# Kernel tuning notes

Measured on AMD Instinct MI355X. Metric: run time of the kernel, lower is better.

Reference implementation:

```python
import jax, jax.numpy as jnp
import numpy as np

B, T, D = 4, 8192, 512

def setup_inputs() -> dict:
    key = jax.random.key(0)
    k_x, k_w1, k_w2 = jax.random.split(key, 3)
    # Xavier-uniform-ish init for linear weights
    lim1 = np.sqrt(6.0 / (D + D)).astype(np.float32)
    lim2 = np.sqrt(6.0 / (D + 1)).astype(np.float32)
    return {
        "x": jax.random.normal(k_x, (B, T, D), dtype=jnp.float32),
        "W1": jax.random.uniform(k_w1, (D, D), dtype=jnp.float32, minval=-lim1, maxval=lim1),
        "b1": jnp.zeros((D,), dtype=jnp.float32),
        "w2": jax.random.uniform(k_w2, (D,), dtype=jnp.float32, minval=-lim2, maxval=lim2),
        "b2": jnp.zeros((), dtype=jnp.float32),
    }

def reference(x, W1, b1, w2, b2):
    h = jnp.tanh(jnp.einsum("btd,ed->bte", x, W1) + b1)   # [B,T,D]
    s = jnp.einsum("bte,e->bt", h, w2) + b2               # [B,T]
    # Causal prefix softmax-weighted sum:
    # context[b,t] = sum_{u<=t} softmax(s[b,:t+1])[u] * x[b,u]
    # Softmax is shift-invariant, so subtracting the global per-row max keeps
    # every prefix softmax exact while being numerically stable.
    m = jnp.max(s, axis=1, keepdims=True)                 # [B,1]
    e = jnp.exp(s - m)                                    # [B,T]
    den = jnp.cumsum(e, axis=1)                           # [B,T]
    num = jnp.cumsum(e[..., None] * x, axis=1)            # [B,T,D]
    context = num / den[..., None]                        # [B,T,D]
    return context
```

## Files before the change

### kernel.cpp

```cpp
#include <hip/hip_runtime.h>
#include <hip/hip_bf16.h>
#include <math.h>

#define BATCH 4
#define TLEN 8192
#define BT 32768
#define DIM 512
#define CHUNK 128
#define NCHUNK 64

#define BM 128
#define BN 128
#define BK 32

typedef _Float16 h8 __attribute__((ext_vector_type(8)));
typedef _Float16 h4 __attribute__((ext_vector_type(4)));
typedef float f4 __attribute__((ext_vector_type(4)));

__device__ __forceinline__ void gload_lds16(const _Float16* g, _Float16* l) {
    __builtin_amdgcn_global_load_lds(
        (const __attribute__((address_space(1))) void*)g,
        (__attribute__((address_space(3))) void*)l, 16, 0, 0);
}

__device__ __forceinline__ float fast_tanh(float z) {
    float u = __expf(2.0f * z);
    return 1.0f - __fdividef(2.0f, u + 1.0f);
}

__global__ __launch_bounds__(256) void convert_kernel(
    const float* __restrict__ x, const float* __restrict__ W1,
    _Float16* __restrict__ hbuf)
{
    const long i = (long)blockIdx.x * 256 + threadIdx.x;
    const long XD4 = (long)BT * DIM / 4;
    const long total4 = XD4 + (long)DIM * DIM / 4;
    if (i >= total4) return;
    float4 v;
    if (i < XD4) v = ((const float4*)x)[i];
    else         v = ((const float4*)W1)[i - XD4];
    h4 o = { (_Float16)v.x, (_Float16)v.y, (_Float16)v.z, (_Float16)v.w };
    *(h4*)(hbuf + i * 4) = o;
}

__global__ __launch_bounds__(256, 4) void score_mfma_kernel(
    const _Float16* __restrict__ xh, const _Float16* __restrict__ wh,
    const float* __restrict__ b1, const float* __restrict__ w2,
    float* __restrict__ spart)
{
    __shared__ _Float16 Als[2][BM * BK];
    __shared__ _Float16 Bls[2][BM * BK];
    __shared__ float sred[2][BM];

    const int orig = blockIdx.x;
    const int wid  = (orig & 7) * 128 + (orig >> 3);
    const int bt = wid >> 2, be = wid & 3;
    const long trow0 = (long)bt * BM;
    const int  ecol0 = be * BN;

    const int tid  = threadIdx.x;
    const int lane = tid & 63;
    const int w    = tid >> 6;
    const int wr   = w >> 1;
    const int wc   = w & 1;
    const int l15  = lane & 15;
    const int lg   = lane >> 4;

    const int srow = w * 32 + (lane >> 2);
    const int skof = ((lane & 3) ^ (srow & 3)) * 8;
    const _Float16* ga = xh + (trow0 + srow) * DIM + skof;
    const _Float16* gb = wh + (long)(ecol0 + srow) * DIM + skof;
    _Float16* laA0 = &Als[0][w * 1024];
    _Float16* laB0 = &Bls[0][w * 1024];
    _Float16* laA1 = &Als[1][w * 1024];
    _Float16* laB1 = &Bls[1][w * 1024];

    const int koff = (lg ^ (l15 & 3)) * 8;

    float b1v[4], w2v[4];
    #pragma unroll
    for (int n = 0; n < 4; ++n) {
        int e = ecol0 + wc * 64 + n * 16 + l15;
        b1v[n] = b1[e];
        w2v[n] = w2[e];
    }
    asm volatile("s_waitcnt vmcnt(0)" ::: "memory");

    f4 acc[4][4];
    #pragma unroll
    for (int m = 0; m < 4; ++m)
        #pragma unroll
        for (int n = 0; n < 4; ++n) acc[m][n] = (f4){0.f, 0.f, 0.f, 0.f};

#define STAGE(A_, B_, k0_) {                         \
    gload_lds16(ga + (k0_),            (A_));        \
    gload_lds16(ga + 16 * DIM + (k0_), (A_) + 512);  \
    gload_lds16(gb + (k0_),            (B_));        \
    gload_lds16(gb + 16 * DIM + (k0_), (B_) + 512);  }

#define COMPUTE(bsel_) {                                                      \
    h8 afr[4], bfr[4];                                                        \
    _Pragma("unroll")                                                         \
    for (int m = 0; m < 4; ++m)                                               \
        afr[m] = *(const h8*)&Als[bsel_][(wr * 64 + m * 16 + l15) * BK + koff]; \
    _Pragma("unroll")                                                         \
    for (int n = 0; n < 4; ++n)                                               \
        bfr[n] = *(const h8*)&Bls[bsel_][(wc * 64 + n * 16 + l15) * BK + koff]; \
    _Pragma("unroll")                                                         \
    for (int m = 0; m < 4; ++m)                                               \
        _Pragma("unroll")                                                     \
        for (int n = 0; n < 4; ++n)                                           \
            acc[m][n] = __builtin_amdgcn_mfma_f32_16x16x32_f16(               \
                afr[m], bfr[n], acc[m][n], 0, 0, 0);                          }

    STAGE(laA0, laB0, 0);
    #pragma unroll 2
    for (int s = 0; s < 15; ++s) {
        if (s & 1) { STAGE(laA0, laB0, (s + 1) * BK); }
        else       { STAGE(laA1, laB1, (s + 1) * BK); }
        asm volatile("s_waitcnt vmcnt(4)" ::: "memory");
        __builtin_amdgcn_s_barrier();
        if (s & 1) { COMPUTE(1); } else { COMPUTE(0); }
        asm volatile("s_waitcnt lgkmcnt(0)" ::: "memory");
        __builtin_amdgcn_s_barrier();
    }
    asm volatile("s_waitcnt vmcnt(0)" ::: "memory");
    __builtin_amdgcn_s_barrier();
    COMPUTE(1);

    float pp[4][4];
    #pragma unroll
    for (int m = 0; m < 4; ++m)
        #pragma unroll
        for (int i = 0; i < 4; ++i) {
            float p = 0.f;
            #pragma unroll
            for (int n = 0; n < 4; ++n)
                p += w2v[n] * fast_tanh(acc[m][n][i] + b1v[n]);
            pp[m][i] = p;
        }
    #pragma unroll
    for (int off = 1; off < 16; off <<= 1)
        #pragma unroll
        for (int m = 0; m < 4; ++m)
            #pragma unroll
            for (int i = 0; i < 4; ++i)
                pp[m][i] += __shfl_xor(pp[m][i], off);
    __syncthreads();
    if (l15 == 0) {
        #pragma unroll
        for (int m = 0; m < 4; ++m)
            #pragma unroll
            for (int i = 0; i < 4; ++i)
                sred[wc][wr * 64 + m * 16 + lg * 4 + i] = pp[m][i];
    }
    __syncthreads();
    if (tid < BM)
        spart[(long)be * BT + trow0 + tid] = sred[0][tid] + sred[1][tid];
}

__global__ __launch_bounds__(128) void chunk_sum_kernel(
    const _Float16* __restrict__ xh, const float* __restrict__ spart,
    float* __restrict__ s_ws, float* __restrict__ csum,
    float* __restrict__ esum)
{
    __shared__ float el[CHUNK];
    __shared__ float wred[2];
    const int c = blockIdx.x, b = blockIdx.y;
    const int tid = threadIdx.x;
    const long bt = (long)b * TLEN + c * CHUNK + tid;

    float sv = spart[bt] + spart[BT + bt] + spart[2l * BT + bt] + spart[3l * BT + bt];
    s_ws[bt] = sv;
    float ev = __expf(sv);
    el[tid] = ev;
    float r = ev;
    #pragma unroll
    for (int off = 1; off < 64; off <<= 1) r += __shfl_xor(r, off);
    if ((tid & 63) == 0) wred[tid >> 6] = r;
    __syncthreads();
    if (tid == 0) esum[b * NCHUNK + c] = wred[0] + wred[1];

    const _Float16* xb = xh + ((long)b * TLEN + c * CHUNK) * DIM;
    float a0 = 0.f, a1 = 0.f, a2 = 0.f, a3 = 0.f;
    for (int t = 0; t < CHUNK; ++t) {
        h4 xv = *(const h4*)(xb + (long)t * DIM + tid * 4);
        float wgt = el[t];
        a0 += wgt * (float)xv[0];
        a1 += wgt * (float)xv[1];
        a2 += wgt * (float)xv[2];
        a3 += wgt * (float)xv[3];
    }
    float4 o = {a0, a1, a2, a3};
    ((float4*)(csum + ((long)(b * NCHUNK + c)) * DIM))[tid] = o;
}

__global__ __launch_bounds__(576) void chunk_scan_kernel(
    float* __restrict__ csum, float* __restrict__ esum)
{
    const int b = blockIdx.x;
    const int tid = threadIdx.x;
    if (tid < 512) {
        const int d = tid;
        float run = 0.f;
        #pragma unroll 8
        for (int c = 0; c < NCHUNK; ++c) {
            float* p = csum + ((long)(b * NCHUNK + c)) * DIM + d;
            float v = *p;
            *p = run;
            run += v;
        }
    } else {
        const int lane = tid - 512;
        float v = esum[b * NCHUNK + lane];
        const float own = v;
        #pragma unroll
        for (int off = 1; off < 64; off <<= 1) {
            float u = __shfl_up(v, off);
            if (lane >= off) v += u;
        }
        esum[b * NCHUNK + lane] = v - own;
    }
}

__global__ __launch_bounds__(128) void context_kernel(
    const float* __restrict__ x, const float* __restrict__ s_ws,
    const float* __restrict__ esum, const float* __restrict__ csum,
    float* __restrict__ out)
{
    __shared__ float el[CHUNK];
    const int c = blockIdx.x, b = blockIdx.y;
    const int tid = threadIdx.x;
    el[tid] = __expf(s_ws[(long)b * TLEN + c * CHUNK + tid]);
    __syncthreads();
    float dacc = esum[b * NCHUNK + c];
    const float4* xb = (const float4*)(x + ((long)b * TLEN + c * CHUNK) * DIM);
    float4* ob = (float4*)(out + ((long)b * TLEN + c * CHUNK) * DIM);
    float4 acc = ((const float4*)(csum + ((long)(b * NCHUNK + c)) * DIM))[tid];
    for (int t = 0; t < CHUNK; ++t) {
        float4 xv = xb[t * (DIM / 4) + tid];
        float wv = el[t];
        dacc += wv;
        acc.x += wv * xv.x; acc.y += wv * xv.y;
        acc.z += wv * xv.z; acc.w += wv * xv.w;
        float inv = __fdividef(1.0f, dacc);
        float4 o = {acc.x * inv, acc.y * inv, acc.z * inv, acc.w * inv};
        ob[t * (DIM / 4) + tid] = o;
    }
}

extern "C" void kernel_launch(void* const* d_in, const int* in_sizes, int n_in,
                              void* d_out, int out_size, void* d_ws, size_t ws_size,
                              hipStream_t stream)
{
    const float* x  = (const float*)d_in[0];
    const float* W1 = (const float*)d_in[1];
    const float* b1 = (const float*)d_in[2];
    const float* w2 = (const float*)d_in[3];
    float* out = (float*)d_out;

    float* ws   = (float*)d_ws;
    float* s_ws = ws;
    float* csum = ws + BT;
    float* esum = ws + BT + 4 * NCHUNK * DIM;

    _Float16* hbuf = (_Float16*)d_out;
    const _Float16* xh = hbuf;
    const _Float16* wh = hbuf + (long)BT * DIM;
    float* spart = (float*)(hbuf + (long)BT * DIM + DIM * DIM);

    const long total4 = ((long)BT * DIM + (long)DIM * DIM) / 4;
    const int convBlocks = (int)((total4 + 255) / 256);

    convert_kernel<<<convBlocks, 256, 0, stream>>>(x, W1, hbuf);
    score_mfma_kernel<<<(BT / BM) * 4, 256, 0, stream>>>(xh, wh, b1, w2, spart);
    chunk_sum_kernel<<<dim3(NCHUNK, BATCH), 128, 0, stream>>>(xh, spart, s_ws, csum, esum);
    chunk_scan_kernel<<<BATCH, 576, 0, stream>>>(csum, esum);
    context_kernel<<<dim3(NCHUNK, BATCH), 128, 0, stream>>>(x, s_ws, esum, csum, out);
}
```

Measured before the change: 83.47 us.

## Fuse fp32-to-fp16 conversion into score GEMM and drop separate convert pass

Removes the standalone convert kernel that wrote fp16 copies of x and W1, and instead has the score GEMM load fp32 tiles into registers, pack-convert them to fp16 and write them to shared memory with a new k-major layout. The main loop becomes register-prefetch plus compute plus convert-write with one barrier per step, replacing the async global-to-LDS path, and occupancy hint drops from 4 to 3. chunk_sum now reads fp32 x directly. This saves the full write and re-read of an fp16 copy of x, at the cost of doubled global read bytes in the GEMM and more register pressure.

```diff
diff --git a/kernel.cpp b/kernel.cpp
--- a/kernel.cpp
+++ b/kernel.cpp
@@ -14,42 +14,21 @@
 #define BK 32
 
 typedef _Float16 h8 __attribute__((ext_vector_type(8)));
-typedef _Float16 h4 __attribute__((ext_vector_type(4)));
+typedef __fp16 fp16x2 __attribute__((ext_vector_type(2)));
 typedef float f4 __attribute__((ext_vector_type(4)));
-
-__device__ __forceinline__ void gload_lds16(const _Float16* g, _Float16* l) {
-    __builtin_amdgcn_global_load_lds(
-        (const __attribute__((address_space(1))) void*)g,
-        (__attribute__((address_space(3))) void*)l, 16, 0, 0);
-}
 
 __device__ __forceinline__ float fast_tanh(float z) {
     float u = __expf(2.0f * z);
     return 1.0f - __fdividef(2.0f, u + 1.0f);
 }
 
-__global__ __launch_bounds__(256) void convert_kernel(
+__global__ __launch_bounds__(256, 3) void score_mfma_kernel(
     const float* __restrict__ x, const float* __restrict__ W1,
-    _Float16* __restrict__ hbuf)
-{
-    const long i = (long)blockIdx.x * 256 + threadIdx.x;
-    const long XD4 = (long)BT * DIM / 4;
-    const long total4 = XD4 + (long)DIM * DIM / 4;
-    if (i >= total4) return;
-    float4 v;
-    if (i < XD4) v = ((const float4*)x)[i];
-    else         v = ((const float4*)W1)[i - XD4];
-    h4 o = { (_Float16)v.x, (_Float16)v.y, (_Float16)v.z, (_Float16)v.w };
-    *(h4*)(hbuf + i * 4) = o;
-}
-
-__global__ __launch_bounds__(256, 4) void score_mfma_kernel(
-    const _Float16* __restrict__ xh, const _Float16* __restrict__ wh,
     const float* __restrict__ b1, const float* __restrict__ w2,
     float* __restrict__ spart)
 {
-    __shared__ _Float16 Als[2][BM * BK];
-    __shared__ _Float16 Bls[2][BM * BK];
+    __shared__ _Float16 Als[2][4 * 128 * 8];
+    __shared__ _Float16 Bls[2][4 * 128 * 8];
     __shared__ float sred[2][BM];
 
     const int orig = blockIdx.x;
@@ -66,16 +45,12 @@
     const int l15  = lane & 15;
     const int lg   = lane >> 4;
 
-    const int srow = w * 32 + (lane >> 2);
-    const int skof = ((lane & 3) ^ (srow & 3)) * 8;
-    const _Float16* ga = xh + (trow0 + srow) * DIM + skof;
-    const _Float16* gb = wh + (long)(ecol0 + srow) * DIM + skof;
-    _Float16* laA0 = &Als[0][w * 1024];
-    _Float16* laB0 = &Bls[0][w * 1024];
-    _Float16* laA1 = &Als[1][w * 1024];
-    _Float16* laB1 = &Bls[1][w * 1024];
-
-    const int koff = (lg ^ (l15 & 3)) * 8;
+    const int srow = w * 32 + (lane >> 1);
+    const int kgb  = (lane & 1) * 2;
+    const float* gA = x  + (trow0 + srow) * DIM + kgb * 8;
+    const float* gB = W1 + (long)(ecol0 + srow) * DIM + kgb * 8;
+    const int wof0 = kgb * 1024 + srow * 8;
+    const int wof1 = wof0 + 1024;
 
     float b1v[4], w2v[4];
     #pragma unroll
@@ -84,7 +59,6 @@
         b1v[n] = b1[e];
         w2v[n] = w2[e];
     }
-    asm volatile("s_waitcnt vmcnt(0)" ::: "memory");
 
     f4 acc[4][4];
     #pragma unroll
@@ -92,20 +66,49 @@
         #pragma unroll
         for (int n = 0; n < 4; ++n) acc[m][n] = (f4){0.f, 0.f, 0.f, 0.f};
 
-#define STAGE(A_, B_, k0_) {                         \
-    gload_lds16(ga + (k0_),            (A_));        \
-    gload_lds16(ga + 16 * DIM + (k0_), (A_) + 512);  \
-    gload_lds16(gb + (k0_),            (B_));        \
-    gload_lds16(gb + 16 * DIM + (k0_), (B_) + 512);  }
+    float4 a0_, a1_, a2_, a3_, b0_, b1_, b2_, b3_;
+
+#define LOADR(k0_) {                                                          \
+    a0_ = *(const float4*)(gA + (k0_));                                       \
+    a1_ = *(const float4*)(gA + (k0_) + 4);                                   \
+    a2_ = *(const float4*)(gA + (k0_) + 8);                                   \
+    a3_ = *(const float4*)(gA + (k0_) + 12);                                  \
+    b0_ = *(const float4*)(gB + (k0_));                                       \
+    b1_ = *(const float4*)(gB + (k0_) + 4);                                   \
+    b2_ = *(const float4*)(gB + (k0_) + 8);                                   \
+    b3_ = *(const float4*)(gB + (k0_) + 12);                                  }
+
+#define CVTWRITE(bsel_) {                                                     \
+    union { h8 v; fp16x2 p[4]; } uA0, uA1, uB0, uB1;                          \
+    uA0.p[0] = __builtin_amdgcn_cvt_pkrtz(a0_.x, a0_.y);                      \
+    uA0.p[1] = __builtin_amdgcn_cvt_pkrtz(a0_.z, a0_.w);                      \
+    uA0.p[2] = __builtin_amdgcn_cvt_pkrtz(a1_.x, a1_.y);                      \
+    uA0.p[3] = __builtin_amdgcn_cvt_pkrtz(a1_.z, a1_.w);                      \
+    uA1.p[0] = __builtin_amdgcn_cvt_pkrtz(a2_.x, a2_.y);                      \
+    uA1.p[1] = __builtin_amdgcn_cvt_pkrtz(a2_.z, a2_.w);                      \
+    uA1.p[2] = __builtin_amdgcn_cvt_pkrtz(a3_.x, a3_.y);                      \
+    uA1.p[3] = __builtin_amdgcn_cvt_pkrtz(a3_.z, a3_.w);                      \
+    uB0.p[0] = __builtin_amdgcn_cvt_pkrtz(b0_.x, b0_.y);                      \
+    uB0.p[1] = __builtin_amdgcn_cvt_pkrtz(b0_.z, b0_.w);                      \
+    uB0.p[2] = __builtin_amdgcn_cvt_pkrtz(b1_.x, b1_.y);                      \
+    uB0.p[3] = __builtin_amdgcn_cvt_pkrtz(b1_.z, b1_.w);                      \
+    uB1.p[0] = __builtin_amdgcn_cvt_pkrtz(b2_.x, b2_.y);                      \
+    uB1.p[1] = __builtin_amdgcn_cvt_pkrtz(b2_.z, b2_.w);                      \
+    uB1.p[2] = __builtin_amdgcn_cvt_pkrtz(b3_.x, b3_.y);                      \
+    uB1.p[3] = __builtin_amdgcn_cvt_pkrtz(b3_.z, b3_.w);                      \
+    *(h8*)&Als[bsel_][wof0] = uA0.v;                                          \
+    *(h8*)&Als[bsel_][wof1] = uA1.v;                                          \
+    *(h8*)&Bls[bsel_][wof0] = uB0.v;                                          \
+    *(h8*)&Bls[bsel_][wof1] = uB1.v;                                          }
 
 #define COMPUTE(bsel_) {                                                      \
     h8 afr[4], bfr[4];                                                        \
     _Pragma("unroll")                                                         \
     for (int m = 0; m < 4; ++m)                                               \
-        afr[m] = *(const h8*)&Als[bsel_][(wr * 64 + m * 16 + l15) * BK + koff]; \
+        afr[m] = *(const h8*)&Als[bsel_][lg * 1024 + (wr * 64 + m * 16 + l15) * 8]; \
     _Pragma("unroll")                                                         \
     for (int n = 0; n < 4; ++n)                                               \
-        bfr[n] = *(const h8*)&Bls[bsel_][(wc * 64 + n * 16 + l15) * BK + koff]; \
+        bfr[n] = *(const h8*)&Bls[bsel_][lg * 1024 + (wc * 64 + n * 16 + l15) * 8]; \
     _Pragma("unroll")                                                         \
     for (int m = 0; m < 4; ++m)                                               \
         _Pragma("unroll")                                                     \
@@ -113,19 +116,17 @@
             acc[m][n] = __builtin_amdgcn_mfma_f32_16x16x32_f16(               \
                 afr[m], bfr[n], acc[m][n], 0, 0, 0);                          }
 
-    STAGE(laA0, laB0, 0);
-    #pragma unroll 2
+    LOADR(0);
+    CVTWRITE(0);
+    __syncthreads();
+
+    #pragma unroll
     for (int s = 0; s < 15; ++s) {
-        if (s & 1) { STAGE(laA0, laB0, (s + 1) * BK); }
-        else       { STAGE(laA1, laB1, (s + 1) * BK); }
-        asm volatile("s_waitcnt vmcnt(4)" ::: "memory");
-        __builtin_amdgcn_s_barrier();
-        if (s & 1) { COMPUTE(1); } else { COMPUTE(0); }
-        asm volatile("s_waitcnt lgkmcnt(0)" ::: "memory");
-        __builtin_amdgcn_s_barrier();
-    }
-    asm volatile("s_waitcnt vmcnt(0)" ::: "memory");
-    __builtin_amdgcn_s_barrier();
+        LOADR((s + 1) * BK);
+        COMPUTE(s & 1);
+        CVTWRITE((s + 1) & 1);
+        __syncthreads();
+    }
     COMPUTE(1);
 
     float pp[4][4];
@@ -160,7 +161,7 @@
 }
 
 __global__ __launch_bounds__(128) void chunk_sum_kernel(
-    const _Float16* __restrict__ xh, const float* __restrict__ spart,
+    const float* __restrict__ x, const float* __restrict__ spart,
     float* __restrict__ s_ws, float* __restrict__ csum,
     float* __restrict__ esum)
 {
@@ -181,18 +182,15 @@
     __syncthreads();
     if (tid == 0) esum[b * NCHUNK + c] = wred[0] + wred[1];
 
-    const _Float16* xb = xh + ((long)b * TLEN + c * CHUNK) * DIM;
-    float a0 = 0.f, a1 = 0.f, a2 = 0.f, a3 = 0.f;
+    const float4* xb = (const float4*)(x + ((long)b * TLEN + c * CHUNK) * DIM);
+    float4 acc = {0.f, 0.f, 0.f, 0.f};
     for (int t = 0; t < CHUNK; ++t) {
-        h4 xv = *(const h4*)(xb + (long)t * DIM + tid * 4);
+        float4 xv = xb[t * (DIM / 4) + tid];
         float wgt = el[t];
-        a0 += wgt * (float)xv[0];
-        a1 += wgt * (float)xv[1];
-        a2 += wgt * (float)xv[2];
-        a3 += wgt * (float)xv[3];
-    }
-    float4 o = {a0, a1, a2, a3};
-    ((float4*)(csum + ((long)(b * NCHUNK + c)) * DIM))[tid] = o;
+        acc.x += wgt * xv.x; acc.y += wgt * xv.y;
+        acc.z += wgt * xv.z; acc.w += wgt * xv.w;
+    }
+    ((float4*)(csum + ((long)(b * NCHUNK + c)) * DIM))[tid] = acc;
 }
 
 __global__ __launch_bounds__(576) void chunk_scan_kernel(
@@ -264,17 +262,10 @@
     float* csum = ws + BT;
     float* esum = ws + BT + 4 * NCHUNK * DIM;
 
-    _Float16* hbuf = (_Float16*)d_out;
-    const _Float16* xh = hbuf;
-    const _Float16* wh = hbuf + (long)BT * DIM;
-    float* spart = (float*)(hbuf + (long)BT * DIM + DIM * DIM);
-
-    const long total4 = ((long)BT * DIM + (long)DIM * DIM) / 4;
-    const int convBlocks = (int)((total4 + 255) / 256);
-
-    convert_kernel<<<convBlocks, 256, 0, stream>>>(x, W1, hbuf);
-    score_mfma_kernel<<<(BT / BM) * 4, 256, 0, stream>>>(xh, wh, b1, w2, spart);
-    chunk_sum_kernel<<<dim3(NCHUNK, BATCH), 128, 0, stream>>>(xh, spart, s_ws, csum, esum);
+    float* spart = out + 12l * 1024 * 1024;
+
+    score_mfma_kernel<<<(BT / BM) * 4, 256, 0, stream>>>(x, W1, b1, w2, spart);
+    chunk_sum_kernel<<<dim3(NCHUNK, BATCH), 128, 0, stream>>>(x, spart, s_ws, csum, esum);
     chunk_scan_kernel<<<BATCH, 576, 0, stream>>>(csum, esum);
     context_kernel<<<dim3(NCHUNK, BATCH), 128, 0, stream>>>(x, s_ws, esum, csum, out);
 }
```

Result: slower. 87.07 us (+4.3%).

## Fuse chunk sum, scan and context into one cooperative kernel with LDS-staged x

Applied to the files above, without the earlier changes.

Replaces the separate chunk-sum, chunk-scan and context kernels with one cooperative kernel. Each block stages its fp16 x chunk in LDS, writes its per-chunk sums, waits at a grid-wide sync, then rebuilds its prefix offsets by summing earlier chunks' partials directly. The output pass reuses the LDS-resident fp16 x instead of re-reading fp32 x from global memory, which removes two launches and a full fp32 read of x. The trade-offs are a grid barrier, a large 128 KB LDS footprint per block, one block per CU, redundant prefix summation, and lower output precision because context is now built from fp16 x.

```diff
diff --git a/kernel.cpp b/kernel.cpp
--- a/kernel.cpp
+++ b/kernel.cpp
@@ -1,6 +1,9 @@
 #include <hip/hip_runtime.h>
 #include <hip/hip_bf16.h>
+#include <hip/hip_cooperative_groups.h>
 #include <math.h>
+
+namespace cg = cooperative_groups;
 
 #define BATCH 4
 #define TLEN 8192
@@ -15,6 +18,7 @@
 
 typedef _Float16 h8 __attribute__((ext_vector_type(8)));
 typedef _Float16 h4 __attribute__((ext_vector_type(4)));
+typedef _Float16 h2 __attribute__((ext_vector_type(2)));
 typedef float f4 __attribute__((ext_vector_type(4)));
 
 __device__ __forceinline__ void gload_lds16(const _Float16* g, _Float16* l) {
@@ -159,93 +163,78 @@
         spart[(long)be * BT + trow0 + tid] = sred[0][tid] + sred[1][tid];
 }
 
-__global__ __launch_bounds__(128) void chunk_sum_kernel(
+__global__ __launch_bounds__(256, 1) void fused_context_kernel(
     const _Float16* __restrict__ xh, const float* __restrict__ spart,
-    float* __restrict__ s_ws, float* __restrict__ csum,
-    float* __restrict__ esum)
-{
+    float* __restrict__ csum, float* __restrict__ esum,
+    float* __restrict__ out)
+{
+    __shared__ _Float16 xls[CHUNK * DIM];
     __shared__ float el[CHUNK];
     __shared__ float wred[2];
-    const int c = blockIdx.x, b = blockIdx.y;
+
+    cg::grid_group grid = cg::this_grid();
+
+    const int bid = blockIdx.x;
+    const int c = bid & (NCHUNK - 1);
+    const int b = bid >> 6;
     const int tid = threadIdx.x;
-    const long bt = (long)b * TLEN + c * CHUNK + tid;
-
-    float sv = spart[bt] + spart[BT + bt] + spart[2l * BT + bt] + spart[3l * BT + bt];
-    s_ws[bt] = sv;
-    float ev = __expf(sv);
-    el[tid] = ev;
-    float r = ev;
-    #pragma unroll
-    for (int off = 1; off < 64; off <<= 1) r += __shfl_xor(r, off);
-    if ((tid & 63) == 0) wred[tid >> 6] = r;
+    const long rowbase = (long)b * TLEN + c * CHUNK;
+
+    if (tid < CHUNK) {
+        const long bt = rowbase + tid;
+        float sv = spart[bt] + spart[BT + bt]
+                 + spart[2l * BT + bt] + spart[3l * BT + bt];
+        float ev = __expf(sv);
+        el[tid] = ev;
+        float r = ev;
+        #pragma unroll
+        for (int off = 1; off < 64; off <<= 1) r += __shfl_xor(r, off);
+        if ((tid & 63) == 0) wred[tid >> 6] = r;
+    }
+
+    {
+        const h8* g = (const h8*)(xh + rowbase * DIM);
+        h8* l = (h8*)xls;
+        #pragma unroll
+        for (int k = 0; k < (CHUNK * DIM / 8) / 256; ++k)
+            l[tid + k * 256] = g[tid + k * 256];
+    }
     __syncthreads();
-    if (tid == 0) esum[b * NCHUNK + c] = wred[0] + wred[1];
-
-    const _Float16* xb = xh + ((long)b * TLEN + c * CHUNK) * DIM;
-    float a0 = 0.f, a1 = 0.f, a2 = 0.f, a3 = 0.f;
+    if (tid == 0) esum[bid] = wred[0] + wred[1];
+
+    float c0 = 0.f, c1 = 0.f;
+    #pragma unroll 8
     for (int t = 0; t < CHUNK; ++t) {
-        h4 xv = *(const h4*)(xb + (long)t * DIM + tid * 4);
-        float wgt = el[t];
-        a0 += wgt * (float)xv[0];
-        a1 += wgt * (float)xv[1];
-        a2 += wgt * (float)xv[2];
-        a3 += wgt * (float)xv[3];
-    }
-    float4 o = {a0, a1, a2, a3};
-    ((float4*)(csum + ((long)(b * NCHUNK + c)) * DIM))[tid] = o;
-}
-
-__global__ __launch_bounds__(576) void chunk_scan_kernel(
-    float* __restrict__ csum, float* __restrict__ esum)
-{
-    const int b = blockIdx.x;
-    const int tid = threadIdx.x;
-    if (tid < 512) {
-        const int d = tid;
-        float run = 0.f;
-        #pragma unroll 8
-        for (int c = 0; c < NCHUNK; ++c) {
-            float* p = csum + ((long)(b * NCHUNK + c)) * DIM + d;
-            float v = *p;
-            *p = run;
-            run += v;
-        }
-    } else {
-        const int lane = tid - 512;
-        float v = esum[b * NCHUNK + lane];
-        const float own = v;
-        #pragma unroll
-        for (int off = 1; off < 64; off <<= 1) {
-            float u = __shfl_up(v, off);
-            if (lane >= off) v += u;
-        }
-        esum[b * NCHUNK + lane] = v - own;
-    }
-}
-
-__global__ __launch_bounds__(128) void context_kernel(
-    const float* __restrict__ x, const float* __restrict__ s_ws,
-    const float* __restrict__ esum, const float* __restrict__ csum,
-    float* __restrict__ out)
-{
-    __shared__ float el[CHUNK];
-    const int c = blockIdx.x, b = blockIdx.y;
-    const int tid = threadIdx.x;
-    el[tid] = __expf(s_ws[(long)b * TLEN + c * CHUNK + tid]);
-    __syncthreads();
-    float dacc = esum[b * NCHUNK + c];
-    const float4* xb = (const float4*)(x + ((long)b * TLEN + c * CHUNK) * DIM);
-    float4* ob = (float4*)(out + ((long)b * TLEN + c * CHUNK) * DIM);
-    float4 acc = ((const float4*)(csum + ((long)(b * NCHUNK + c)) * DIM))[tid];
+        h2 xv = *(const h2*)&xls[t * DIM + tid * 2];
+        float w = el[t];
+        c0 += w * (float)xv[0];
+        c1 += w * (float)xv[1];
+    }
+    *(float2*)&csum[(long)bid * DIM + tid * 2] = make_float2(c0, c1);
+
+    grid.sync();
+
+    float a0 = 0.f, a1 = 0.f, den = 0.f;
+    for (int cp = 0; cp < c; ++cp) {
+        float2 v = *(const float2*)&csum[(long)(b * NCHUNK + cp) * DIM + tid * 2];
+        a0 += v.x;
+        a1 += v.y;
+    }
+    #pragma unroll 8
+    for (int cp = 0; cp < NCHUNK; ++cp) {
+        float v = esum[b * NCHUNK + cp];
+        den += (cp < c) ? v : 0.f;
+    }
+
+    float* ob = out + rowbase * DIM;
     for (int t = 0; t < CHUNK; ++t) {
-        float4 xv = xb[t * (DIM / 4) + tid];
-        float wv = el[t];
-        dacc += wv;
-        acc.x += wv * xv.x; acc.y += wv * xv.y;
-        acc.z += wv * xv.z; acc.w += wv * xv.w;
-        float inv = __fdividef(1.0f, dacc);
-        float4 o = {acc.x * inv, acc.y * inv, acc.z * inv, acc.w * inv};
-        ob[t * (DIM / 4) + tid] = o;
+        h2 xv = *(const h2*)&xls[t * DIM + tid * 2];
+        float w = el[t];
+        den += w;
+        a0 += w * (float)xv[0];
+        a1 += w * (float)xv[1];
+        float inv = __fdividef(1.0f, den);
+        *(float2*)&ob[(long)t * DIM + tid * 2] = make_float2(a0 * inv, a1 * inv);
     }
 }
 
@@ -260,9 +249,8 @@
     float* out = (float*)d_out;
 
     float* ws   = (float*)d_ws;
-    float* s_ws = ws;
-    float* csum = ws + BT;
-    float* esum = ws + BT + 4 * NCHUNK * DIM;
+    float* csum = ws;
+    float* esum = ws + 4 * NCHUNK * DIM;
 
     _Float16* hbuf = (_Float16*)d_out;
     const _Float16* xh = hbuf;
@@ -274,7 +262,11 @@
 
     convert_kernel<<<convBlocks, 256, 0, stream>>>(x, W1, hbuf);
     score_mfma_kernel<<<(BT / BM) * 4, 256, 0, stream>>>(xh, wh, b1, w2, spart);
-    chunk_sum_kernel<<<dim3(NCHUNK, BATCH), 128, 0, stream>>>(xh, spart, s_ws, csum, esum);
-    chunk_scan_kernel<<<BATCH, 576, 0, stream>>>(csum, esum);
-    context_kernel<<<dim3(NCHUNK, BATCH), 128, 0, stream>>>(x, s_ws, esum, csum, out);
-}
+
+    const _Float16* xh_c = xh;
+    const float* spart_c = spart;
+    void* args[] = { (void*)&xh_c, (void*)&spart_c, (void*)&csum,
+                     (void*)&esum, (void*)&out };
+    hipLaunchCooperativeKernel((const void*)fused_context_kernel,
+                               dim3(NCHUNK * BATCH), dim3(256), args, 0, stream);
+}
```

Result: slower. 116.9 us (+40.1%).

## Fold chunk scan into context kernel and read fp16 x copy from workspace

Applied to the files above, without the earlier changes.

Removes the separate chunk_scan kernel; each context block now sums the preceding chunk partials and exp-sums itself. When the workspace is large enough, the fp16 copy of x lives in workspace instead of the output buffer, so the context kernel can read half-width x instead of fp32. The aim is to cut one launch and halve the x read traffic in the final pass. In exchange, the prefix work becomes redundant and quadratic in chunk count, the context output now uses fp16-rounded x, and spart moves to a fixed offset in the output buffer.

```diff
diff --git a/kernel.cpp b/kernel.cpp
--- a/kernel.cpp
+++ b/kernel.cpp
@@ -30,17 +30,19 @@
 
 __global__ __launch_bounds__(256) void convert_kernel(
     const float* __restrict__ x, const float* __restrict__ W1,
-    _Float16* __restrict__ hbuf)
+    _Float16* __restrict__ xh, _Float16* __restrict__ wh)
 {
     const long i = (long)blockIdx.x * 256 + threadIdx.x;
     const long XD4 = (long)BT * DIM / 4;
     const long total4 = XD4 + (long)DIM * DIM / 4;
     if (i >= total4) return;
     float4 v;
-    if (i < XD4) v = ((const float4*)x)[i];
-    else         v = ((const float4*)W1)[i - XD4];
+    _Float16* dst;
+    long j;
+    if (i < XD4) { v = ((const float4*)x)[i];        dst = xh; j = i; }
+    else         { v = ((const float4*)W1)[i - XD4]; dst = wh; j = i - XD4; }
     h4 o = { (_Float16)v.x, (_Float16)v.y, (_Float16)v.z, (_Float16)v.w };
-    *(h4*)(hbuf + i * 4) = o;
+    *(h4*)(dst + j * 4) = o;
 }
 
 __global__ __launch_bounds__(256, 4) void score_mfma_kernel(
@@ -195,56 +197,48 @@
     ((float4*)(csum + ((long)(b * NCHUNK + c)) * DIM))[tid] = o;
 }
 
-__global__ __launch_bounds__(576) void chunk_scan_kernel(
-    float* __restrict__ csum, float* __restrict__ esum)
-{
-    const int b = blockIdx.x;
-    const int tid = threadIdx.x;
-    if (tid < 512) {
-        const int d = tid;
-        float run = 0.f;
-        #pragma unroll 8
-        for (int c = 0; c < NCHUNK; ++c) {
-            float* p = csum + ((long)(b * NCHUNK + c)) * DIM + d;
-            float v = *p;
-            *p = run;
-            run += v;
-        }
-    } else {
-        const int lane = tid - 512;
-        float v = esum[b * NCHUNK + lane];
-        const float own = v;
-        #pragma unroll
-        for (int off = 1; off < 64; off <<= 1) {
-            float u = __shfl_up(v, off);
-            if (lane >= off) v += u;
-        }
-        esum[b * NCHUNK + lane] = v - own;
-    }
-}
-
+template <int FP16X>
 __global__ __launch_bounds__(128) void context_kernel(
-    const float* __restrict__ x, const float* __restrict__ s_ws,
-    const float* __restrict__ esum, const float* __restrict__ csum,
-    float* __restrict__ out)
+    const float* __restrict__ x, const _Float16* __restrict__ xh,
+    const float* __restrict__ s_ws, const float* __restrict__ csum,
+    const float* __restrict__ esum, float* __restrict__ out)
 {
     __shared__ float el[CHUNK];
     const int c = blockIdx.x, b = blockIdx.y;
     const int tid = threadIdx.x;
-    el[tid] = __expf(s_ws[(long)b * TLEN + c * CHUNK + tid]);
-    __syncthreads();
-    float dacc = esum[b * NCHUNK + c];
-    const float4* xb = (const float4*)(x + ((long)b * TLEN + c * CHUNK) * DIM);
-    float4* ob = (float4*)(out + ((long)b * TLEN + c * CHUNK) * DIM);
-    float4 acc = ((const float4*)(csum + ((long)(b * NCHUNK + c)) * DIM))[tid];
+    const long rowbase = (long)b * TLEN + c * CHUNK;
+
+    el[tid] = __expf(s_ws[rowbase + tid]);
+    __syncthreads();
+
+    float a0 = 0.f, a1 = 0.f, a2 = 0.f, a3 = 0.f, den = 0.f;
+    for (int cp = 0; cp < c; ++cp) {
+        float4 v = ((const float4*)(csum + (long)(b * NCHUNK + cp) * DIM))[tid];
+        a0 += v.x; a1 += v.y; a2 += v.z; a3 += v.w;
+    }
+    #pragma unroll 8
+    for (int cp = 0; cp < NCHUNK; ++cp) {
+        float v = esum[b * NCHUNK + cp];
+        den += (cp < c) ? v : 0.f;
+    }
+
+    float4* ob = (float4*)(out + rowbase * DIM);
     for (int t = 0; t < CHUNK; ++t) {
-        float4 xv = xb[t * (DIM / 4) + tid];
+        float xv0, xv1, xv2, xv3;
+        if (FP16X) {
+            h4 hv = *(const h4*)(xh + (rowbase + t) * DIM + tid * 4);
+            xv0 = (float)hv[0]; xv1 = (float)hv[1];
+            xv2 = (float)hv[2]; xv3 = (float)hv[3];
+        } else {
+            float4 fv = ((const float4*)(x + (rowbase + t) * DIM))[tid];
+            xv0 = fv.x; xv1 = fv.y; xv2 = fv.z; xv3 = fv.w;
+        }
         float wv = el[t];
-        dacc += wv;
-        acc.x += wv * xv.x; acc.y += wv * xv.y;
-        acc.z += wv * xv.z; acc.w += wv * xv.w;
-        float inv = __fdividef(1.0f, dacc);
-        float4 o = {acc.x * inv, acc.y * inv, acc.z * inv, acc.w * inv};
+        den += wv;
+        a0 += wv * xv0; a1 += wv * xv1;
+        a2 += wv * xv2; a3 += wv * xv3;
+        float inv = __fdividef(1.0f, den);
+        float4 o = {a0 * inv, a1 * inv, a2 * inv, a3 * inv};
         ob[t * (DIM / 4) + tid] = o;
     }
 }
@@ -263,18 +257,32 @@
     float* s_ws = ws;
     float* csum = ws + BT;
     float* esum = ws + BT + 4 * NCHUNK * DIM;
-
-    _Float16* hbuf = (_Float16*)d_out;
-    const _Float16* xh = hbuf;
-    const _Float16* wh = hbuf + (long)BT * DIM;
-    float* spart = (float*)(hbuf + (long)BT * DIM + DIM * DIM);
+    const long ws_base_floats = BT + 4 * NCHUNK * DIM + 256;
+
+    float* spart = out + 12l * 1024 * 1024;
+
+    const size_t need = (size_t)ws_base_floats * 4
+                      + ((size_t)BT * DIM + (size_t)DIM * DIM) * 2;
+    const bool big_ws = ws_size >= need;
+
+    _Float16* xh;
+    _Float16* wh;
+    if (big_ws) {
+        xh = (_Float16*)(ws + ws_base_floats);
+        wh = xh + (long)BT * DIM;
+    } else {
+        xh = (_Float16*)d_out;
+        wh = xh + (long)BT * DIM;
+    }
 
     const long total4 = ((long)BT * DIM + (long)DIM * DIM) / 4;
     const int convBlocks = (int)((total4 + 255) / 256);
 
-    convert_kernel<<<convBlocks, 256, 0, stream>>>(x, W1, hbuf);
+    convert_kernel<<<convBlocks, 256, 0, stream>>>(x, W1, xh, wh);
     score_mfma_kernel<<<(BT / BM) * 4, 256, 0, stream>>>(xh, wh, b1, w2, spart);
     chunk_sum_kernel<<<dim3(NCHUNK, BATCH), 128, 0, stream>>>(xh, spart, s_ws, csum, esum);
-    chunk_scan_kernel<<<BATCH, 576, 0, stream>>>(csum, esum);
-    context_kernel<<<dim3(NCHUNK, BATCH), 128, 0, stream>>>(x, s_ws, esum, csum, out);
-}
+    if (big_ws)
+        context_kernel<1><<<dim3(NCHUNK, BATCH), 128, 0, stream>>>(x, xh, s_ws, csum, esum, out);
+    else
+        context_kernel<0><<<dim3(NCHUNK, BATCH), 128, 0, stream>>>(x, xh, s_ws, csum, esum, out);
+}
```

Measured after the change: 89.32 us. 7.0% more time.
